# Kernel optimization log

Hardware: AMD Instinct MI355X
Metric: run time of the kernel (lower is better)

The kernel has to match this reference:

```python
import jax, jax.numpy as jnp
import numpy as np

B, S, L, D, E, VOCAB = 256, 32, 32, 256, 64, 50000
EPS = 1e-12  # tf.math.l2_normalize epsilon


def setup_inputs() -> dict:
    key = jax.random.key(0)
    ks = jax.random.split(key, 6)
    first_prgrph = jax.random.randint(ks[0], (B, S, L), 0, VOCAB, dtype=jnp.int32)
    p1_mask = jnp.ones((B, S, L), jnp.float32)
    entity_keys = jax.random.normal(ks[1], (B, E, D), jnp.float32)
    embedding_matrix = jax.random.normal(ks[2], (VOCAB, D), jnp.float32) * 0.02
    U = jax.random.normal(ks[3], (D, D), jnp.float32) * 0.05
    V = jax.random.normal(ks[4], (D, D), jnp.float32) * 0.05
    W = jax.random.normal(ks[5], (D, D), jnp.float32) * 0.05
    return dict(first_prgrph=first_prgrph, p1_mask=p1_mask, entity_keys=entity_keys,
                embedding_matrix=embedding_matrix, U=U, V=V, W=W)


def reference(first_prgrph, p1_mask, entity_keys, embedding_matrix, U, V, W):
    # Sentence encoder: masked bag-of-words sum over words.  [B,S,D]
    emb = embedding_matrix[first_prgrph] * p1_mask[..., None]  # [B,S,L,D]
    enc = jnp.sum(emb, axis=2)                                 # [B,S,D]
    sent_active = p1_mask.sum(axis=2) > 0                      # [B,S] which sentences exist

    hiddens0 = jnp.zeros_like(entity_keys)                     # [B,E,D]

    def step(h, inp):
        e, active = inp  # e: [B,D], active: [B]
        eb = e[:, None, :]                                     # [B,1,D]
        # gate g_i = sigmoid(<e, h_i> + <e, k_i>)              # [B,E]
        g = jax.nn.sigmoid(jnp.sum(eb * h + eb * entity_keys, axis=2))
        # h_tilda = relu(hU + kV + eW)                         # [B,E,D]
        h_t = jax.nn.relu(h @ U + entity_keys @ V + (e @ W)[:, None, :])
        h_new = h + g[..., None] * h_t
        # l2 normalize along entity embedding dim (tf.math.l2_normalize semantics)
        sq = jnp.sum(h_new * h_new, axis=2, keepdims=True)
        h_new = h_new * jax.lax.rsqrt(jnp.maximum(sq, EPS))
        h = jnp.where(active[:, None, None], h_new, h)
        return h, None

    h_final, _ = jax.lax.scan(
        step, hiddens0,
        (jnp.swapaxes(enc, 0, 1), jnp.swapaxes(sent_active, 0, 1)))  # scan over S
    return h_final  # [B,E,D] final entity memories
```

## Files before the change

kernel.cpp:

```cpp
#include <hip/hip_runtime.h>
#include <hip/hip_bf16.h>

#define Bb 256
#define Ss 32
#define Ll 32
#define Dd 256
#define Ee 64

typedef __attribute__((ext_vector_type(8))) short short8v;
typedef __attribute__((ext_vector_type(4))) float float4v;

static __device__ __forceinline__ unsigned short f2bf(float f) {
    unsigned int x = __float_as_uint(f);
    return (unsigned short)((x + 0x7fffu + ((x >> 16) & 1u)) >> 16);
}
static __device__ __forceinline__ unsigned int pk2(float a, float b) {
    return (unsigned int)f2bf(a) | ((unsigned int)f2bf(b) << 16);
}

__global__ void k_enc(const int* __restrict__ tok, const float* __restrict__ mask,
                      const float* __restrict__ emb, float* __restrict__ enc,
                      int* __restrict__ act) {
    int bs = blockIdx.x;
    int d  = threadIdx.x;
    const int*   t = tok  + (long)bs * Ll;
    const float* m = mask + (long)bs * Ll;
    float acc = 0.f;
    #pragma unroll 4
    for (int l = 0; l < Ll; ++l) {
        acc += emb[(long)t[l] * Dd + d] * m[l];
    }
    enc[(long)bs * Dd + d] = acc;
    if (d == 0) {
        float s = 0.f;
        for (int l = 0; l < Ll; ++l) s += m[l];
        act[bs] = (s > 0.f) ? 1 : 0;
    }
}

__global__ void k_rowmat(const float* __restrict__ X, const float* __restrict__ M,
                         float* __restrict__ Y) {
    __shared__ __align__(16) float xs[16 * Dd];
    int tid = threadIdx.x;
    long row0 = (long)blockIdx.x * 16;
    #pragma unroll
    for (int i = 0; i < 16; ++i) xs[i * Dd + tid] = X[(row0 + i) * Dd + tid];
    __syncthreads();
    int cg = tid & 63;
    int rq = tid >> 6;
    float acc[4][4];
    #pragma unroll
    for (int r = 0; r < 4; ++r)
        #pragma unroll
        for (int c = 0; c < 4; ++c) acc[r][c] = 0.f;
    for (int d = 0; d < Dd; ++d) {
        float4 mv = *reinterpret_cast<const float4*>(&M[d * Dd + cg * 4]);
        #pragma unroll
        for (int r = 0; r < 4; ++r) {
            float x = xs[(rq * 4 + r) * Dd + d];
            acc[r][0] += x * mv.x; acc[r][1] += x * mv.y;
            acc[r][2] += x * mv.z; acc[r][3] += x * mv.w;
        }
    }
    #pragma unroll
    for (int r = 0; r < 4; ++r) {
        float4 o = make_float4(acc[r][0], acc[r][1], acc[r][2], acc[r][3]);
        *reinterpret_cast<float4*>(&Y[(row0 + rq * 4 + r) * Dd + cg * 4]) = o;
    }
}

__global__ __launch_bounds__(256) void k_gk(const float* __restrict__ enc,
                                            const float* __restrict__ keys,
                                            float* __restrict__ gk) {
    __shared__ __align__(16) char kls[Ee * 1024];
    __shared__ __align__(16) float es[Ss * Dd];
    const int tid = threadIdx.x;
    const int b   = blockIdx.x;
    {
        const float4* kg = reinterpret_cast<const float4*>(keys + (long)b * Ee * Dd);
        #pragma unroll
        for (int i = 0; i < 16; ++i) {
            const int idx = tid + 256 * i;
            const int e   = idx >> 6;
            const int d4  = idx & 63;
            *reinterpret_cast<float4*>(kls + (((e << 10) + (d4 << 4)) ^ ((e & 7) << 4)))
                = kg[idx];
        }
        const float4* eg = reinterpret_cast<const float4*>(enc + (long)b * Ss * Dd);
        float4* es4 = reinterpret_cast<float4*>(es);
        #pragma unroll
        for (int i = 0; i < 8; ++i) es4[tid + 256 * i] = eg[tid + 256 * i];
    }
    __syncthreads();
    const int w = tid >> 6;
    const int e = tid & 63;
    float acc[8];
    #pragma unroll
    for (int i = 0; i < 8; ++i) acc[i] = 0.f;
    const char* krow = kls;
    for (int d4 = 0; d4 < 64; ++d4) {
        const float4 kvf = *reinterpret_cast<const float4*>(
            krow + (((e << 10) + (d4 << 4)) ^ ((e & 7) << 4)));
        #pragma unroll
        for (int i = 0; i < 8; ++i) {
            const float4 ev = *reinterpret_cast<const float4*>(&es[(w * 8 + i) * Dd + d4 * 4]);
            acc[i] += ev.x * kvf.x + ev.y * kvf.y + ev.z * kvf.z + ev.w * kvf.w;
        }
    }
    #pragma unroll
    for (int i = 0; i < 8; ++i)
        gk[((long)b * Ss + w * 8 + i) * Ee + e] = acc[i];
}

__global__ void k_ut(const float* __restrict__ U, unsigned short* __restrict__ Utg) {
    const int c0 = blockIdx.x * 16;
    const int k  = threadIdx.x;
    float v[16];
    #pragma unroll
    for (int i = 0; i < 16; ++i) v[i] = U[k * Dd + c0 + i];
    #pragma unroll
    for (int i = 0; i < 16; ++i) Utg[(c0 + i) * Dd + k] = f2bf(v[i]);
}

__global__ __launch_bounds__(512, 1) void k_scan(
    const float* __restrict__ enc, const int* __restrict__ act,
    const float* __restrict__ gk,  const float* __restrict__ kv,
    const float* __restrict__ eWm, const unsigned short* __restrict__ Utg,
    float* __restrict__ out) {
    __shared__ __align__(16) unsigned short hbf[Ee * Dd];
    __shared__ float part_g[8][Ee];
    __shared__ float part_rn[8][Ee];

    const int tid = threadIdx.x;
    const int b   = blockIdx.x;
    const int w   = tid >> 6;
    const int l   = tid & 63;
    const int q   = l >> 4;
    const int sl  = l & 15;
    const int c0  = w * 32;

    {
        uint4 z4 = make_uint4(0u, 0u, 0u, 0u);
        uint4* hz = reinterpret_cast<uint4*>(hbf);
        #pragma unroll
        for (int i = 0; i < 4; ++i) hz[tid + 512 * i] = z4;
        (&part_g[0][0])[tid]  = 0.f;
        (&part_rn[0][0])[tid] = 0.f;
    }

    short8v aU[2][8];
    #pragma unroll
    for (int mi = 0; mi < 2; ++mi)
        #pragma unroll
        for (int kk = 0; kk < 8; ++kk)
            aU[mi][kk] = *reinterpret_cast<const short8v*>(
                Utg + (c0 + mi * 16 + sl) * Dd + kk * 32 + q * 8);

    float4v kvr[2][4];
    #pragma unroll
    for (int mi = 0; mi < 2; ++mi)
        #pragma unroll
        for (int n = 0; n < 4; ++n)
            kvr[mi][n] = *reinterpret_cast<const float4v*>(
                kv + ((long)b * Ee + n * 16 + sl) * Dd + c0 + mi * 16 + q * 4);

    float4v h_d[2][4];
    #pragma unroll
    for (int mi = 0; mi < 2; ++mi)
        #pragma unroll
        for (int n = 0; n < 4; ++n) h_d[mi][n] = (float4v)0.f;

    const unsigned long long actmask = __ballot((l < Ss) && (act[b * Ss + l] != 0));
    const int bswz = (sl & 7) << 4;
    char* hb = reinterpret_cast<char*>(hbf);

    float4v esN[2];
    #pragma unroll
    for (int mi = 0; mi < 2; ++mi)
        esN[mi] = *reinterpret_cast<const float4v*>(
            enc + (long)(b * Ss) * Dd + c0 + mi * 16 + q * 4);

    __syncthreads();

    for (int s = 0; s < Ss; ++s) {
        const long bs = (long)b * Ss + s;
        float4v esc[2] = {esN[0], esN[1]};
        if (s + 1 < Ss) {
            #pragma unroll
            for (int mi = 0; mi < 2; ++mi)
                esN[mi] = *reinterpret_cast<const float4v*>(
                    enc + (bs + 1) * Dd + c0 + mi * 16 + q * 4);
        }
        if ((actmask >> s) & 1ull) {
            float gkl[4];
            #pragma unroll
            for (int n = 0; n < 4; ++n) gkl[n] = gk[bs * Ee + n * 16 + sl];

            #pragma unroll
            for (int n = 0; n < 4; ++n) {
                float pg = esc[0][0] * h_d[0][n][0] + esc[0][1] * h_d[0][n][1]
                         + esc[0][2] * h_d[0][n][2] + esc[0][3] * h_d[0][n][3]
                         + esc[1][0] * h_d[1][n][0] + esc[1][1] * h_d[1][n][1]
                         + esc[1][2] * h_d[1][n][2] + esc[1][3] * h_d[1][n][3];
                pg += __shfl_xor(pg, 16);
                pg += __shfl_xor(pg, 32);
                if (q == 0) part_g[w][n * 16 + sl] = pg;
            }
            __syncthreads();

            float g4[4];
            #pragma unroll
            for (int n = 0; n < 4; ++n) {
                const int e = n * 16 + sl;
                float x = part_g[0][e] + part_g[1][e] + part_g[2][e] + part_g[3][e]
                        + part_g[4][e] + part_g[5][e] + part_g[6][e] + part_g[7][e]
                        + gkl[n];
                g4[n] = 1.f / (1.f + expf(-x));
            }

            float4v acc[2][4];
            #pragma unroll
            for (int mi = 0; mi < 2; ++mi)
                #pragma unroll
                for (int n = 0; n < 4; ++n) acc[mi][n] = (float4v)0.f;
            #pragma unroll
            for (int kk = 0; kk < 8; ++kk) {
                short8v bh[4];
                #pragma unroll
                for (int n = 0; n < 4; ++n)
                    bh[n] = *reinterpret_cast<const short8v*>(
                        hb + ((((n * 16 + sl) << 9) + (kk << 6) + (q << 4)) ^ bswz));
                #pragma unroll
                for (int mi = 0; mi < 2; ++mi)
                    #pragma unroll
                    for (int n = 0; n < 4; ++n)
                        acc[mi][n] = __builtin_amdgcn_mfma_f32_16x16x32_bf16(
                            aU[mi][kk], bh[n], acc[mi][n], 0, 0, 0);
            }

            const float* ewrow = eWm + bs * Dd + c0;
            float ssp[4];
            #pragma unroll
            for (int n = 0; n < 4; ++n) {
                float sp = 0.f;
                #pragma unroll
                for (int mi = 0; mi < 2; ++mi) {
                    const float4v ew = *reinterpret_cast<const float4v*>(
                        ewrow + mi * 16 + q * 4);
                    #pragma unroll
                    for (int j = 0; j < 4; ++j) {
                        float ht = acc[mi][n][j] + kvr[mi][n][j] + ew[j];
                        ht = fmaxf(ht, 0.f);
                        const float hn = h_d[mi][n][j] + g4[n] * ht;
                        h_d[mi][n][j] = hn;
                        sp += hn * hn;
                    }
                }
                ssp[n] = sp;
            }
            #pragma unroll
            for (int n = 0; n < 4; ++n) {
                ssp[n] += __shfl_xor(ssp[n], 16);
                ssp[n] += __shfl_xor(ssp[n], 32);
                if (q == 0) part_rn[w][n * 16 + sl] = ssp[n];
            }
            __syncthreads();

            #pragma unroll
            for (int n = 0; n < 4; ++n) {
                const int e = n * 16 + sl;
                const float t = part_rn[0][e] + part_rn[1][e] + part_rn[2][e]
                              + part_rn[3][e] + part_rn[4][e] + part_rn[5][e]
                              + part_rn[6][e] + part_rn[7][e];
                const float rn = rsqrtf(fmaxf(t, 1e-12f));
                #pragma unroll
                for (int mi = 0; mi < 2; ++mi) {
                    h_d[mi][n][0] *= rn; h_d[mi][n][1] *= rn;
                    h_d[mi][n][2] *= rn; h_d[mi][n][3] *= rn;
                    const int c = c0 + mi * 16 + q * 4;
                    const unsigned int u0 = pk2(h_d[mi][n][0], h_d[mi][n][1]);
                    const unsigned int u1 = pk2(h_d[mi][n][2], h_d[mi][n][3]);
                    *reinterpret_cast<uint2*>(hb + (((e << 9) + (c << 1)) ^ bswz))
                        = make_uint2(u0, u1);
                }
            }
        }
    }

    #pragma unroll
    for (int mi = 0; mi < 2; ++mi)
        #pragma unroll
        for (int n = 0; n < 4; ++n)
            *reinterpret_cast<float4v*>(
                out + ((long)b * Ee + n * 16 + sl) * Dd + c0 + mi * 16 + q * 4)
                = h_d[mi][n];
}

extern "C" void kernel_launch(void* const* d_in, const int* in_sizes, int n_in,
                              void* d_out, int out_size, void* d_ws, size_t ws_size,
                              hipStream_t stream) {
    const int*   tok  = (const int*)d_in[0];
    const float* mask = (const float*)d_in[1];
    const float* keys = (const float*)d_in[2];
    const float* emb  = (const float*)d_in[3];
    const float* U    = (const float*)d_in[4];
    const float* V    = (const float*)d_in[5];
    const float* W    = (const float*)d_in[6];
    float* out = (float*)d_out;

    float* enc = (float*)d_ws;
    float* kv  = enc + (long)Bb * Ss * Dd;
    float* eW  = kv  + (long)Bb * Ee * Dd;
    float* gkv = eW  + (long)Bb * Ss * Dd;
    int*   act = (int*)(gkv + (long)Bb * Ss * Ee);
    unsigned short* Utg = (unsigned short*)(act + Bb * Ss);

    k_enc<<<Bb * Ss, Dd, 0, stream>>>(tok, mask, emb, enc, act);
    k_rowmat<<<(Bb * Ee) / 16, 256, 0, stream>>>(keys, V, kv);
    k_rowmat<<<(Bb * Ss) / 16, 256, 0, stream>>>(enc, W, eW);
    k_gk<<<Bb, 256, 0, stream>>>(enc, keys, gkv);
    k_ut<<<Dd / 16, Dd, 0, stream>>>(U, Utg);
    k_scan<<<Bb, 512, 0, stream>>>(enc, act, gkv, kv, eW, Utg, out);
}
```

Before: 460.4 us.

## Split scan work across 16 waves per batch with 16 columns each

The recurrent scan kernel now launches 1024 threads per batch element, so each of 16 waves owns 16 output columns instead of 32. Per-wave MFMA work and register state are halved, and the cross-wave reductions for the gate and the norm grow to 16 partials. The kv tile is no longer held in registers for the whole scan and is instead reloaded from global memory at every step, trading register pressure for extra memory traffic. The aim is to shorten the serial per-step latency of the scan by spreading it over more waves, at the cost of more expensive barriers.

```diff
diff --git a/kernel.cpp b/kernel.cpp
--- a/kernel.cpp
+++ b/kernel.cpp
@@ -122,14 +122,14 @@
     for (int i = 0; i < 16; ++i) Utg[(c0 + i) * Dd + k] = f2bf(v[i]);
 }
 
-__global__ __launch_bounds__(512, 1) void k_scan(
+__global__ __launch_bounds__(1024, 1) void k_scan(
     const float* __restrict__ enc, const int* __restrict__ act,
     const float* __restrict__ gk,  const float* __restrict__ kv,
     const float* __restrict__ eWm, const unsigned short* __restrict__ Utg,
     float* __restrict__ out) {
     __shared__ __align__(16) unsigned short hbf[Ee * Dd];
-    __shared__ float part_g[8][Ee];
-    __shared__ float part_rn[8][Ee];
+    __shared__ float part_g[16][Ee];
+    __shared__ float part_rn[16][Ee];
 
     const int tid = threadIdx.x;
     const int b   = blockIdx.x;
@@ -137,60 +137,42 @@
     const int l   = tid & 63;
     const int q   = l >> 4;
     const int sl  = l & 15;
-    const int c0  = w * 32;
+    const int c0  = w * 16;
 
     {
         uint4 z4 = make_uint4(0u, 0u, 0u, 0u);
         uint4* hz = reinterpret_cast<uint4*>(hbf);
         #pragma unroll
-        for (int i = 0; i < 4; ++i) hz[tid + 512 * i] = z4;
+        for (int i = 0; i < 2; ++i) hz[tid + 1024 * i] = z4;
         (&part_g[0][0])[tid]  = 0.f;
         (&part_rn[0][0])[tid] = 0.f;
     }
 
-    short8v aU[2][8];
-    #pragma unroll
-    for (int mi = 0; mi < 2; ++mi)
-        #pragma unroll
-        for (int kk = 0; kk < 8; ++kk)
-            aU[mi][kk] = *reinterpret_cast<const short8v*>(
-                Utg + (c0 + mi * 16 + sl) * Dd + kk * 32 + q * 8);
-
-    float4v kvr[2][4];
-    #pragma unroll
-    for (int mi = 0; mi < 2; ++mi)
-        #pragma unroll
-        for (int n = 0; n < 4; ++n)
-            kvr[mi][n] = *reinterpret_cast<const float4v*>(
-                kv + ((long)b * Ee + n * 16 + sl) * Dd + c0 + mi * 16 + q * 4);
-
-    float4v h_d[2][4];
-    #pragma unroll
-    for (int mi = 0; mi < 2; ++mi)
-        #pragma unroll
-        for (int n = 0; n < 4; ++n) h_d[mi][n] = (float4v)0.f;
+    short8v aU[8];
+    #pragma unroll
+    for (int kk = 0; kk < 8; ++kk)
+        aU[kk] = *reinterpret_cast<const short8v*>(
+            Utg + (c0 + sl) * Dd + kk * 32 + q * 8);
+
+    float4v h_d[4];
+    #pragma unroll
+    for (int n = 0; n < 4; ++n) h_d[n] = (float4v)0.f;
 
     const unsigned long long actmask = __ballot((l < Ss) && (act[b * Ss + l] != 0));
     const int bswz = (sl & 7) << 4;
     char* hb = reinterpret_cast<char*>(hbf);
 
-    float4v esN[2];
-    #pragma unroll
-    for (int mi = 0; mi < 2; ++mi)
-        esN[mi] = *reinterpret_cast<const float4v*>(
-            enc + (long)(b * Ss) * Dd + c0 + mi * 16 + q * 4);
+    float4v esN = *reinterpret_cast<const float4v*>(
+        enc + (long)(b * Ss) * Dd + c0 + q * 4);
 
     __syncthreads();
 
     for (int s = 0; s < Ss; ++s) {
         const long bs = (long)b * Ss + s;
-        float4v esc[2] = {esN[0], esN[1]};
-        if (s + 1 < Ss) {
-            #pragma unroll
-            for (int mi = 0; mi < 2; ++mi)
-                esN[mi] = *reinterpret_cast<const float4v*>(
-                    enc + (bs + 1) * Dd + c0 + mi * 16 + q * 4);
-        }
+        const float4v esc = esN;
+        if (s + 1 < Ss)
+            esN = *reinterpret_cast<const float4v*>(
+                enc + (bs + 1) * Dd + c0 + q * 4);
         if ((actmask >> s) & 1ull) {
             float gkl[4];
             #pragma unroll
@@ -198,10 +180,8 @@
 
             #pragma unroll
             for (int n = 0; n < 4; ++n) {
-                float pg = esc[0][0] * h_d[0][n][0] + esc[0][1] * h_d[0][n][1]
-                         + esc[0][2] * h_d[0][n][2] + esc[0][3] * h_d[0][n][3]
-                         + esc[1][0] * h_d[1][n][0] + esc[1][1] * h_d[1][n][1]
-                         + esc[1][2] * h_d[1][n][2] + esc[1][3] * h_d[1][n][3];
+                float pg = esc[0] * h_d[n][0] + esc[1] * h_d[n][1]
+                         + esc[2] * h_d[n][2] + esc[3] * h_d[n][3];
                 pg += __shfl_xor(pg, 16);
                 pg += __shfl_xor(pg, 32);
                 if (q == 0) part_g[w][n * 16 + sl] = pg;
@@ -212,17 +192,17 @@
             #pragma unroll
             for (int n = 0; n < 4; ++n) {
                 const int e = n * 16 + sl;
-                float x = part_g[0][e] + part_g[1][e] + part_g[2][e] + part_g[3][e]
-                        + part_g[4][e] + part_g[5][e] + part_g[6][e] + part_g[7][e]
-                        + gkl[n];
+                float x0 = part_g[0][e] + part_g[1][e] + part_g[2][e] + part_g[3][e];
+                float x1 = part_g[4][e] + part_g[5][e] + part_g[6][e] + part_g[7][e];
+                float x2 = part_g[8][e] + part_g[9][e] + part_g[10][e] + part_g[11][e];
+                float x3 = part_g[12][e] + part_g[13][e] + part_g[14][e] + part_g[15][e];
+                const float x = (x0 + x1) + (x2 + x3) + gkl[n];
                 g4[n] = 1.f / (1.f + expf(-x));
             }
 
-            float4v acc[2][4];
-            #pragma unroll
-            for (int mi = 0; mi < 2; ++mi)
-                #pragma unroll
-                for (int n = 0; n < 4; ++n) acc[mi][n] = (float4v)0.f;
+            float4v acc[4];
+            #pragma unroll
+            for (int n = 0; n < 4; ++n) acc[n] = (float4v)0.f;
             #pragma unroll
             for (int kk = 0; kk < 8; ++kk) {
                 short8v bh[4];
@@ -231,30 +211,29 @@
                     bh[n] = *reinterpret_cast<const short8v*>(
                         hb + ((((n * 16 + sl) << 9) + (kk << 6) + (q << 4)) ^ bswz));
                 #pragma unroll
-                for (int mi = 0; mi < 2; ++mi)
-                    #pragma unroll
-                    for (int n = 0; n < 4; ++n)
-                        acc[mi][n] = __builtin_amdgcn_mfma_f32_16x16x32_bf16(
-                            aU[mi][kk], bh[n], acc[mi][n], 0, 0, 0);
-            }
-
-            const float* ewrow = eWm + bs * Dd + c0;
+                for (int n = 0; n < 4; ++n)
+                    acc[n] = __builtin_amdgcn_mfma_f32_16x16x32_bf16(
+                        aU[kk], bh[n], acc[n], 0, 0, 0);
+            }
+
+            const float4v ewv = *reinterpret_cast<const float4v*>(
+                eWm + bs * Dd + c0 + q * 4);
+            float4v kvv[4];
+            #pragma unroll
+            for (int n = 0; n < 4; ++n)
+                kvv[n] = *reinterpret_cast<const float4v*>(
+                    kv + ((long)b * Ee + n * 16 + sl) * Dd + c0 + q * 4);
             float ssp[4];
             #pragma unroll
             for (int n = 0; n < 4; ++n) {
                 float sp = 0.f;
                 #pragma unroll
-                for (int mi = 0; mi < 2; ++mi) {
-                    const float4v ew = *reinterpret_cast<const float4v*>(
-                        ewrow + mi * 16 + q * 4);
-                    #pragma unroll
-                    for (int j = 0; j < 4; ++j) {
-                        float ht = acc[mi][n][j] + kvr[mi][n][j] + ew[j];
-                        ht = fmaxf(ht, 0.f);
-                        const float hn = h_d[mi][n][j] + g4[n] * ht;
-                        h_d[mi][n][j] = hn;
-                        sp += hn * hn;
-                    }
+                for (int j = 0; j < 4; ++j) {
+                    float ht = acc[n][j] + kvv[n][j] + ewv[j];
+                    ht = fmaxf(ht, 0.f);
+                    const float hn = h_d[n][j] + g4[n] * ht;
+                    h_d[n][j] = hn;
+                    sp += hn * hn;
                 }
                 ssp[n] = sp;
             }
@@ -269,31 +248,27 @@
             #pragma unroll
             for (int n = 0; n < 4; ++n) {
                 const int e = n * 16 + sl;
-                const float t = part_rn[0][e] + part_rn[1][e] + part_rn[2][e]
-                              + part_rn[3][e] + part_rn[4][e] + part_rn[5][e]
-                              + part_rn[6][e] + part_rn[7][e];
+                float t0 = part_rn[0][e] + part_rn[1][e] + part_rn[2][e] + part_rn[3][e];
+                float t1 = part_rn[4][e] + part_rn[5][e] + part_rn[6][e] + part_rn[7][e];
+                float t2 = part_rn[8][e] + part_rn[9][e] + part_rn[10][e] + part_rn[11][e];
+                float t3 = part_rn[12][e] + part_rn[13][e] + part_rn[14][e] + part_rn[15][e];
+                const float t = (t0 + t1) + (t2 + t3);
                 const float rn = rsqrtf(fmaxf(t, 1e-12f));
-                #pragma unroll
-                for (int mi = 0; mi < 2; ++mi) {
-                    h_d[mi][n][0] *= rn; h_d[mi][n][1] *= rn;
-                    h_d[mi][n][2] *= rn; h_d[mi][n][3] *= rn;
-                    const int c = c0 + mi * 16 + q * 4;
-                    const unsigned int u0 = pk2(h_d[mi][n][0], h_d[mi][n][1]);
-                    const unsigned int u1 = pk2(h_d[mi][n][2], h_d[mi][n][3]);
-                    *reinterpret_cast<uint2*>(hb + (((e << 9) + (c << 1)) ^ bswz))
-                        = make_uint2(u0, u1);
-                }
-            }
-        }
-    }
-
-    #pragma unroll
-    for (int mi = 0; mi < 2; ++mi)
-        #pragma unroll
-        for (int n = 0; n < 4; ++n)
-            *reinterpret_cast<float4v*>(
-                out + ((long)b * Ee + n * 16 + sl) * Dd + c0 + mi * 16 + q * 4)
-                = h_d[mi][n];
+                h_d[n][0] *= rn; h_d[n][1] *= rn;
+                h_d[n][2] *= rn; h_d[n][3] *= rn;
+                const int c = c0 + q * 4;
+                const unsigned int u0 = pk2(h_d[n][0], h_d[n][1]);
+                const unsigned int u1 = pk2(h_d[n][2], h_d[n][3]);
+                *reinterpret_cast<uint2*>(hb + (((e << 9) + (c << 1)) ^ bswz))
+                    = make_uint2(u0, u1);
+            }
+        }
+    }
+
+    #pragma unroll
+    for (int n = 0; n < 4; ++n)
+        *reinterpret_cast<float4v*>(
+            out + ((long)b * Ee + n * 16 + sl) * Dd + c0 + q * 4) = h_d[n];
 }
 
 extern "C" void kernel_launch(void* const* d_in, const int* in_sizes, int n_in,
@@ -320,5 +295,5 @@
     k_rowmat<<<(Bb * Ss) / 16, 256, 0, stream>>>(enc, W, eW);
     k_gk<<<Bb, 256, 0, stream>>>(enc, keys, gkv);
     k_ut<<<Dd / 16, Dd, 0, stream>>>(U, Utg);
-    k_scan<<<Bb, 512, 0, stream>>>(enc, act, gkv, kv, eW, Utg, out);
-}
+    k_scan<<<Bb, 1024, 0, stream>>>(enc, act, gkv, kv, eW, Utg, out);
+}
```

Result: slower. 853.2 us (+85.3%).

## Retile scan kernel to 2x4 warp grid with U staged in LDS

Applied to the files above, without the earlier changes.

The scan kernel's warps are reorganized into a 2 (entity halves) x 4 (column quarters) grid, so each warp computes 64 columns x 32 entities instead of 32 columns x 64 entities. The cross-warp reductions for gate and norm shrink from 8 to 4 partials. The U^T bf16 operand is no longer held in registers: most of it (224 rows) sits in swizzled LDS, and the last tile is read from global memory each step. The MFMA loop is double-buffered in software, and kv/enc rows are now loaded per step rather than kept in registers. A separate change in the rowmat kernel transposes its LDS tile so each thread fetches its x values with one float4 load.

```diff
diff --git a/kernel.cpp b/kernel.cpp
--- a/kernel.cpp
+++ b/kernel.cpp
@@ -6,6 +6,7 @@
 #define Ll 32
 #define Dd 256
 #define Ee 64
+#define WC_TAIL 224
 
 typedef __attribute__((ext_vector_type(8))) short short8v;
 typedef __attribute__((ext_vector_type(4))) float float4v;
@@ -40,11 +41,11 @@
 
 __global__ void k_rowmat(const float* __restrict__ X, const float* __restrict__ M,
                          float* __restrict__ Y) {
-    __shared__ __align__(16) float xs[16 * Dd];
+    __shared__ __align__(16) float xs_t[Dd * 16];
     int tid = threadIdx.x;
     long row0 = (long)blockIdx.x * 16;
     #pragma unroll
-    for (int i = 0; i < 16; ++i) xs[i * Dd + tid] = X[(row0 + i) * Dd + tid];
+    for (int i = 0; i < 16; ++i) xs_t[tid * 16 + i] = X[(row0 + i) * Dd + tid];
     __syncthreads();
     int cg = tid & 63;
     int rq = tid >> 6;
@@ -55,11 +56,12 @@
         for (int c = 0; c < 4; ++c) acc[r][c] = 0.f;
     for (int d = 0; d < Dd; ++d) {
         float4 mv = *reinterpret_cast<const float4*>(&M[d * Dd + cg * 4]);
+        float4 xv = *reinterpret_cast<const float4*>(&xs_t[d * 16 + rq * 4]);
+        const float xa[4] = {xv.x, xv.y, xv.z, xv.w};
         #pragma unroll
         for (int r = 0; r < 4; ++r) {
-            float x = xs[(rq * 4 + r) * Dd + d];
-            acc[r][0] += x * mv.x; acc[r][1] += x * mv.y;
-            acc[r][2] += x * mv.z; acc[r][3] += x * mv.w;
+            acc[r][0] += xa[r] * mv.x; acc[r][1] += xa[r] * mv.y;
+            acc[r][2] += xa[r] * mv.z; acc[r][3] += xa[r] * mv.w;
         }
     }
     #pragma unroll
@@ -127,9 +129,10 @@
     const float* __restrict__ gk,  const float* __restrict__ kv,
     const float* __restrict__ eWm, const unsigned short* __restrict__ Utg,
     float* __restrict__ out) {
-    __shared__ __align__(16) unsigned short hbf[Ee * Dd];
-    __shared__ float part_g[8][Ee];
-    __shared__ float part_rn[8][Ee];
+    __shared__ __align__(128) unsigned short Uls[WC_TAIL * Dd];
+    __shared__ __align__(128) unsigned short hbf[Ee * Dd];
+    __shared__ float part_g[4][Ee];
+    __shared__ float part_rn[4][Ee];
 
     const int tid = threadIdx.x;
     const int b   = blockIdx.x;
@@ -137,150 +140,158 @@
     const int l   = tid & 63;
     const int q   = l >> 4;
     const int sl  = l & 15;
-    const int c0  = w * 32;
+    const int we  = w & 1;
+    const int wc  = w >> 1;
+    const int e0  = we * 32 + sl;
+    const int c0  = wc * 64;
+    const int bswz = (sl & 7) << 4;
 
     {
         uint4 z4 = make_uint4(0u, 0u, 0u, 0u);
         uint4* hz = reinterpret_cast<uint4*>(hbf);
         #pragma unroll
         for (int i = 0; i < 4; ++i) hz[tid + 512 * i] = z4;
-        (&part_g[0][0])[tid]  = 0.f;
-        (&part_rn[0][0])[tid] = 0.f;
-    }
-
-    short8v aU[2][8];
-    #pragma unroll
-    for (int mi = 0; mi < 2; ++mi)
-        #pragma unroll
-        for (int kk = 0; kk < 8; ++kk)
-            aU[mi][kk] = *reinterpret_cast<const short8v*>(
-                Utg + (c0 + mi * 16 + sl) * Dd + kk * 32 + q * 8);
-
-    float4v kvr[2][4];
-    #pragma unroll
-    for (int mi = 0; mi < 2; ++mi)
-        #pragma unroll
-        for (int n = 0; n < 4; ++n)
-            kvr[mi][n] = *reinterpret_cast<const float4v*>(
-                kv + ((long)b * Ee + n * 16 + sl) * Dd + c0 + mi * 16 + q * 4);
-
-    float4v h_d[2][4];
-    #pragma unroll
-    for (int mi = 0; mi < 2; ++mi)
-        #pragma unroll
-        for (int n = 0; n < 4; ++n) h_d[mi][n] = (float4v)0.f;
+    }
+    {
+        const uint4* g4 = reinterpret_cast<const uint4*>(Utg);
+        char* ub = reinterpret_cast<char*>(Uls);
+        #pragma unroll
+        for (int r = 0; r < 14; ++r) {
+            const int u  = tid + 512 * r;
+            const int c  = u >> 5;
+            const int kb = (u & 31) << 4;
+            *reinterpret_cast<uint4*>(ub + (((c << 9) + kb) ^ ((c & 7) << 4))) = g4[u];
+        }
+    }
 
     const unsigned long long actmask = __ballot((l < Ss) && (act[b * Ss + l] != 0));
-    const int bswz = (sl & 7) << 4;
-    char* hb = reinterpret_cast<char*>(hbf);
-
-    float4v esN[2];
-    #pragma unroll
-    for (int mi = 0; mi < 2; ++mi)
-        esN[mi] = *reinterpret_cast<const float4v*>(
-            enc + (long)(b * Ss) * Dd + c0 + mi * 16 + q * 4);
+
+    float4v h_d[4][2];
+    #pragma unroll
+    for (int mi = 0; mi < 4; ++mi)
+        #pragma unroll
+        for (int n = 0; n < 2; ++n) h_d[mi][n] = (float4v)0.f;
+
+    const char* ub = reinterpret_cast<const char*>(Uls);
+    const char* hc = reinterpret_cast<const char*>(hbf);
 
     __syncthreads();
 
+#define LDA(KK, A) { _Pragma("unroll") for (int mi_ = 0; mi_ < 4; ++mi_) { \
+        const int cc = c0 + mi_ * 16 + sl; \
+        if (c0 + mi_ * 16 >= WC_TAIL) \
+            A[mi_] = *reinterpret_cast<const short8v*>(Utg + cc * Dd + (KK) * 32 + q * 8); \
+        else \
+            A[mi_] = *reinterpret_cast<const short8v*>( \
+                ub + (((cc << 9) + ((KK) << 6) + (q << 4)) ^ ((sl & 7) << 4))); } }
+#define LDB(KK, Bv) { _Pragma("unroll") for (int n_ = 0; n_ < 2; ++n_) { \
+        const int ee = e0 + n_ * 16; \
+        Bv[n_] = *reinterpret_cast<const short8v*>( \
+            hc + (((ee << 9) + ((KK) << 6) + (q << 4)) ^ bswz)); } }
+#define MFMA8(A, Bv) { _Pragma("unroll") for (int mi_ = 0; mi_ < 4; ++mi_) \
+        _Pragma("unroll") for (int n_ = 0; n_ < 2; ++n_) \
+            acc[mi_][n_] = __builtin_amdgcn_mfma_f32_16x16x32_bf16( \
+                A[mi_], Bv[n_], acc[mi_][n_], 0, 0, 0); }
+
     for (int s = 0; s < Ss; ++s) {
-        const long bs = (long)b * Ss + s;
-        float4v esc[2] = {esN[0], esN[1]};
-        if (s + 1 < Ss) {
-            #pragma unroll
-            for (int mi = 0; mi < 2; ++mi)
-                esN[mi] = *reinterpret_cast<const float4v*>(
-                    enc + (bs + 1) * Dd + c0 + mi * 16 + q * 4);
-        }
         if ((actmask >> s) & 1ull) {
-            float gkl[4];
-            #pragma unroll
-            for (int n = 0; n < 4; ++n) gkl[n] = gk[bs * Ee + n * 16 + sl];
-
-            #pragma unroll
-            for (int n = 0; n < 4; ++n) {
-                float pg = esc[0][0] * h_d[0][n][0] + esc[0][1] * h_d[0][n][1]
-                         + esc[0][2] * h_d[0][n][2] + esc[0][3] * h_d[0][n][3]
-                         + esc[1][0] * h_d[1][n][0] + esc[1][1] * h_d[1][n][1]
-                         + esc[1][2] * h_d[1][n][2] + esc[1][3] * h_d[1][n][3];
+            const long bs = (long)b * Ss + s;
+            const float* erow = enc + bs * Dd + c0;
+            float4 esc[4];
+            #pragma unroll
+            for (int mi = 0; mi < 4; ++mi)
+                esc[mi] = *reinterpret_cast<const float4*>(erow + mi * 16 + q * 4);
+            float gkl[2];
+            #pragma unroll
+            for (int n = 0; n < 2; ++n) gkl[n] = gk[bs * Ee + e0 + n * 16];
+
+            #pragma unroll
+            for (int n = 0; n < 2; ++n) {
+                float pg = 0.f;
+                #pragma unroll
+                for (int mi = 0; mi < 4; ++mi) {
+                    pg += esc[mi].x * h_d[mi][n][0] + esc[mi].y * h_d[mi][n][1]
+                        + esc[mi].z * h_d[mi][n][2] + esc[mi].w * h_d[mi][n][3];
+                }
                 pg += __shfl_xor(pg, 16);
                 pg += __shfl_xor(pg, 32);
-                if (q == 0) part_g[w][n * 16 + sl] = pg;
+                if (q == 0) part_g[wc][e0 + n * 16] = pg;
             }
             __syncthreads();
 
-            float g4[4];
-            #pragma unroll
-            for (int n = 0; n < 4; ++n) {
-                const int e = n * 16 + sl;
-                float x = part_g[0][e] + part_g[1][e] + part_g[2][e] + part_g[3][e]
-                        + part_g[4][e] + part_g[5][e] + part_g[6][e] + part_g[7][e]
-                        + gkl[n];
-                g4[n] = 1.f / (1.f + expf(-x));
-            }
-
-            float4v acc[2][4];
-            #pragma unroll
-            for (int mi = 0; mi < 2; ++mi)
+            float g2[2];
+            #pragma unroll
+            for (int n = 0; n < 2; ++n) {
+                const int e = e0 + n * 16;
+                const float x = (part_g[0][e] + part_g[1][e])
+                              + (part_g[2][e] + part_g[3][e]) + gkl[n];
+                g2[n] = 1.f / (1.f + expf(-x));
+            }
+
+            float4v acc[4][2];
+            #pragma unroll
+            for (int mi = 0; mi < 4; ++mi)
                 #pragma unroll
-                for (int n = 0; n < 4; ++n) acc[mi][n] = (float4v)0.f;
-            #pragma unroll
-            for (int kk = 0; kk < 8; ++kk) {
-                short8v bh[4];
+                for (int n = 0; n < 2; ++n) acc[mi][n] = (float4v)0.f;
+
+            short8v A0[4], A1[4], B0[2], B1[2];
+            LDA(0, A0); LDB(0, B0);
+            #pragma unroll
+            for (int kp = 0; kp < 4; ++kp) {
+                LDA(2 * kp + 1, A1); LDB(2 * kp + 1, B1);
+                MFMA8(A0, B0);
+                if (kp < 3) { LDA(2 * kp + 2, A0); LDB(2 * kp + 2, B0); }
+                MFMA8(A1, B1);
+            }
+
+            const float* ewrow = eWm + bs * Dd + c0;
+            float4 eww[4];
+            #pragma unroll
+            for (int mi = 0; mi < 4; ++mi)
+                eww[mi] = *reinterpret_cast<const float4*>(ewrow + mi * 16 + q * 4);
+            float ssp[2] = {0.f, 0.f};
+            #pragma unroll
+            for (int n = 0; n < 2; ++n) {
+                const long krow = ((long)b * Ee + e0 + n * 16) * Dd + c0;
                 #pragma unroll
-                for (int n = 0; n < 4; ++n)
-                    bh[n] = *reinterpret_cast<const short8v*>(
-                        hb + ((((n * 16 + sl) << 9) + (kk << 6) + (q << 4)) ^ bswz));
-                #pragma unroll
-                for (int mi = 0; mi < 2; ++mi)
-                    #pragma unroll
-                    for (int n = 0; n < 4; ++n)
-                        acc[mi][n] = __builtin_amdgcn_mfma_f32_16x16x32_bf16(
-                            aU[mi][kk], bh[n], acc[mi][n], 0, 0, 0);
-            }
-
-            const float* ewrow = eWm + bs * Dd + c0;
-            float ssp[4];
-            #pragma unroll
-            for (int n = 0; n < 4; ++n) {
-                float sp = 0.f;
-                #pragma unroll
-                for (int mi = 0; mi < 2; ++mi) {
-                    const float4v ew = *reinterpret_cast<const float4v*>(
-                        ewrow + mi * 16 + q * 4);
+                for (int mi = 0; mi < 4; ++mi) {
+                    const float4 kvv = *reinterpret_cast<const float4*>(
+                        kv + krow + mi * 16 + q * 4);
+                    const float kva[4] = {kvv.x, kvv.y, kvv.z, kvv.w};
+                    const float ewa[4] = {eww[mi].x, eww[mi].y, eww[mi].z, eww[mi].w};
                     #pragma unroll
                     for (int j = 0; j < 4; ++j) {
-                        float ht = acc[mi][n][j] + kvr[mi][n][j] + ew[j];
+                        float ht = acc[mi][n][j] + kva[j] + ewa[j];
                         ht = fmaxf(ht, 0.f);
-                        const float hn = h_d[mi][n][j] + g4[n] * ht;
+                        const float hn = h_d[mi][n][j] + g2[n] * ht;
                         h_d[mi][n][j] = hn;
-                        sp += hn * hn;
+                        ssp[n] += hn * hn;
                     }
                 }
-                ssp[n] = sp;
-            }
-            #pragma unroll
-            for (int n = 0; n < 4; ++n) {
+            }
+            #pragma unroll
+            for (int n = 0; n < 2; ++n) {
                 ssp[n] += __shfl_xor(ssp[n], 16);
                 ssp[n] += __shfl_xor(ssp[n], 32);
-                if (q == 0) part_rn[w][n * 16 + sl] = ssp[n];
+                if (q == 0) part_rn[wc][e0 + n * 16] = ssp[n];
             }
             __syncthreads();
 
-            #pragma unroll
-            for (int n = 0; n < 4; ++n) {
-                const int e = n * 16 + sl;
-                const float t = part_rn[0][e] + part_rn[1][e] + part_rn[2][e]
-                              + part_rn[3][e] + part_rn[4][e] + part_rn[5][e]
-                              + part_rn[6][e] + part_rn[7][e];
+            char* hw = const_cast<char*>(hc);
+            #pragma unroll
+            for (int n = 0; n < 2; ++n) {
+                const int e = e0 + n * 16;
+                const float t = (part_rn[0][e] + part_rn[1][e])
+                              + (part_rn[2][e] + part_rn[3][e]);
                 const float rn = rsqrtf(fmaxf(t, 1e-12f));
                 #pragma unroll
-                for (int mi = 0; mi < 2; ++mi) {
+                for (int mi = 0; mi < 4; ++mi) {
                     h_d[mi][n][0] *= rn; h_d[mi][n][1] *= rn;
                     h_d[mi][n][2] *= rn; h_d[mi][n][3] *= rn;
-                    const int c = c0 + mi * 16 + q * 4;
+                    const int d0 = c0 + mi * 16 + q * 4;
                     const unsigned int u0 = pk2(h_d[mi][n][0], h_d[mi][n][1]);
                     const unsigned int u1 = pk2(h_d[mi][n][2], h_d[mi][n][3]);
-                    *reinterpret_cast<uint2*>(hb + (((e << 9) + (c << 1)) ^ bswz))
+                    *reinterpret_cast<uint2*>(hw + (((e << 9) + (d0 << 1)) ^ bswz))
                         = make_uint2(u0, u1);
                 }
             }
@@ -288,12 +299,17 @@
     }
 
     #pragma unroll
-    for (int mi = 0; mi < 2; ++mi)
-        #pragma unroll
-        for (int n = 0; n < 4; ++n)
-            *reinterpret_cast<float4v*>(
-                out + ((long)b * Ee + n * 16 + sl) * Dd + c0 + mi * 16 + q * 4)
-                = h_d[mi][n];
+    for (int n = 0; n < 2; ++n)
+        #pragma unroll
+        for (int mi = 0; mi < 4; ++mi) {
+            float4 o = make_float4(h_d[mi][n][0], h_d[mi][n][1],
+                                   h_d[mi][n][2], h_d[mi][n][3]);
+            *reinterpret_cast<float4*>(
+                out + ((long)b * Ee + e0 + n * 16) * Dd + c0 + mi * 16 + q * 4) = o;
+        }
+#undef LDA
+#undef LDB
+#undef MFMA8
 }
 
 extern "C" void kernel_launch(void* const* d_in, const int* in_sizes, int n_in,
```

Result: faster. 399.8 us (-13.2%).
